# Optimization experiments

Measured on AMD Instinct MI355X. Metric: run time of the kernel, lower is better.

Reference implementation:

```python
import jax, jax.numpy as jnp
import numpy as np


def setup_inputs() -> dict:
    key = jax.random.key(0)
    k1, k2 = jax.random.split(key)
    B, S, D_IN, D_OUT = 4, 2048, 2048, 8192
    x = jax.random.normal(k1, (B, S, D_IN), dtype=jnp.float32)
    # kaiming_normal_ fan_out, linear: std = 1/sqrt(fan_out)
    weight = jax.random.normal(k2, (D_OUT, D_IN), dtype=jnp.float32) * (1.0 / np.sqrt(D_OUT))
    return {"x": x, "weight": weight}


def reference(x, weight):
    # Per-output-row mean-abs scale, clamped
    scale = jnp.clip(jnp.mean(jnp.abs(weight), axis=1, keepdims=True), 1e-5, None)  # [out, 1]
    w_q = jnp.clip(jnp.round(weight / scale), -1.0, 1.0)  # ternary {-1, 0, 1}
    # STE: value = w_q * scale, gradient flows to weight as identity
    w = weight + jax.lax.stop_gradient(w_q * scale - weight)  # [out, in]
    # F.linear: x @ w.T
    return jnp.einsum('bsi,oi->bso', x, w)
```

## Files before the change

### kernel.cpp

```cpp
#include <hip/hip_runtime.h>
#include <hip/hip_bf16.h>
#include <stdint.h>


typedef float floatx4 __attribute__((ext_vector_type(4)));
typedef __bf16 bf16x8 __attribute__((ext_vector_type(8)));

#define BM 128
#define BN 128
#define BK 32

__global__ __launch_bounds__(256) void quant_weight(
    const float* __restrict__ W, uint16_t* __restrict__ Q,
    float* __restrict__ scale, int K )
{
    const int o = blockIdx.x;
    const int t = threadIdx.x;
    const float* row = W + (size_t)o * K;
    const float4* row4 = (const float4*)row;

    float4 v0 = row4[t];
    float4 v1 = row4[t + 256];
    float s = fabsf(v0.x) + fabsf(v0.y) + fabsf(v0.z) + fabsf(v0.w)
            + fabsf(v1.x) + fabsf(v1.y) + fabsf(v1.z) + fabsf(v1.w);
    #pragma unroll
    for (int off = 32; off; off >>= 1) s += __shfl_down(s, off, 64);

    __shared__ float partial[4];
    __shared__ float inv_sh;
    if ((t & 63) == 0) partial[t >> 6] = s;
    __syncthreads();
    if (t == 0) {
        float tot = partial[0] + partial[1] + partial[2] + partial[3];
        float sc = fmaxf(tot / (float)K, 1e-5f);
        scale[o] = sc;
        inv_sh = 1.0f / sc;
    }
    __syncthreads();
    const float inv = inv_sh;

    uint16_t* qrow = Q + (size_t)o * K;
    float q0[4] = {v0.x, v0.y, v0.z, v0.w};
    float q1[4] = {v1.x, v1.y, v1.z, v1.w};
    ushort4 o0, o1;
    unsigned short* p0 = (unsigned short*)&o0;
    unsigned short* p1 = (unsigned short*)&o1;
    #pragma unroll
    for (int i = 0; i < 4; ++i) {
        float a = fminf(fmaxf(rintf(q0[i] * inv), -1.f), 1.f);
        float b = fminf(fmaxf(rintf(q1[i] * inv), -1.f), 1.f);
        p0[i] = (unsigned short)(__float_as_uint(a) >> 16);
        p1[i] = (unsigned short)(__float_as_uint(b) >> 16);
    }
    ((ushort4*)qrow)[t] = o0;
    ((ushort4*)qrow)[t + 256] = o1;
}

__global__ __launch_bounds__(256) void cvt_bf16(
    const float* __restrict__ X, uint16_t* __restrict__ Y)
{
    const size_t i = (size_t)blockIdx.x * blockDim.x + threadIdx.x;
    const float4* x4 = (const float4*)X;
    float4 a = x4[2 * i];
    float4 b = x4[2 * i + 1];
    float v[8] = {a.x, a.y, a.z, a.w, b.x, b.y, b.z, b.w};
    ushort4 lo, hi;
    unsigned short* pl = (unsigned short*)&lo;
    unsigned short* ph = (unsigned short*)&hi;
    #pragma unroll
    for (int j = 0; j < 4; ++j) {
        unsigned ua = __float_as_uint(v[j]);
        unsigned ub = __float_as_uint(v[j + 4]);
        pl[j] = (unsigned short)((ua + 0x7fffu + ((ua >> 16) & 1u)) >> 16);
        ph[j] = (unsigned short)((ub + 0x7fffu + ((ub >> 16) & 1u)) >> 16);
    }
    ((ushort4*)Y)[2 * i] = lo;
    ((ushort4*)Y)[2 * i + 1] = hi;
}

__device__ inline void gload_lds16(const void* g, void* l) {
    __builtin_amdgcn_global_load_lds(
        (const __attribute__((address_space(1))) void*)g,
        (__attribute__((address_space(3))) void*)l, 16, 0, 0);
}

__global__ __launch_bounds__(256) void gemm_bt_scaled(
    const uint16_t* __restrict__ A,
    const uint16_t* __restrict__ B,
    const float* __restrict__ scale,
    float* __restrict__ C,
    int M, int N, int K)
{
    __shared__ __align__(16) uint16_t sA[BM * BK];
    __shared__ __align__(16) uint16_t sB[BN * BK];

    const int tid  = threadIdx.x;
    const int lane = tid & 63;
    const int wv   = tid >> 6;
    const int wm   = wv & 1;
    const int wn   = wv >> 1;
    const int bm   = blockIdx.y;
    const int bn   = blockIdx.x;
    const int rowA0 = bm * BM;
    const int rowB0 = bn * BN;

    const int lrow  = lane & 15;
    const int kquad = lane >> 4;
    const int aoff0 = (wm * 64 + lrow) * BK + kquad * 8;
    const int boff0 = (wn * 64 + lrow) * BK + kquad * 8;

    floatx4 acc[4][4] = {};

    for (int kk = 0; kk < K; kk += BK) {
        #pragma unroll
        for (int j = 0; j < 2; ++j) {
            int c = tid + 256 * j;
            const uint16_t* ga = A + (size_t)(rowA0 + (c >> 2)) * K + kk + (c & 3) * 8;
            gload_lds16(ga, &sA[c * 8]);
        }
        #pragma unroll
        for (int j = 0; j < 2; ++j) {
            int c = tid + 256 * j;
            const uint16_t* gb = B + (size_t)(rowB0 + (c >> 2)) * K + kk + (c & 3) * 8;
            gload_lds16(gb, &sB[c * 8]);
        }
        __syncthreads();

        bf16x8 af[4], bfr[4];
        #pragma unroll
        for (int mt = 0; mt < 4; ++mt)
            af[mt] = *(const bf16x8*)&sA[aoff0 + mt * 16 * BK];
        #pragma unroll
        for (int nt = 0; nt < 4; ++nt)
            bfr[nt] = *(const bf16x8*)&sB[boff0 + nt * 16 * BK];

        #pragma unroll
        for (int mt = 0; mt < 4; ++mt)
            #pragma unroll
            for (int nt = 0; nt < 4; ++nt)
                acc[mt][nt] = __builtin_amdgcn_mfma_f32_16x16x32_bf16(
                    af[mt], bfr[nt], acc[mt][nt], 0, 0, 0);
        __syncthreads();
    }

    const int colb = rowB0 + wn * 64 + lrow;
    const int rowb = rowA0 + wm * 64 + kquad * 4;
    #pragma unroll
    for (int nt = 0; nt < 4; ++nt) {
        const float sc = scale[colb + nt * 16];
        #pragma unroll
        for (int mt = 0; mt < 4; ++mt) {
            #pragma unroll
            for (int r = 0; r < 4; ++r) {
                C[(size_t)(rowb + mt * 16 + r) * N + colb + nt * 16] =
                    acc[mt][nt][r] * sc;
            }
        }
    }
}

extern "C" void kernel_launch(void* const* d_in, const int* in_sizes, int n_in,
                              void* d_out, int out_size, void* d_ws, size_t ws_size,
                              hipStream_t stream) {
    const float* x = (const float*)d_in[0];
    const float* w = (const float*)d_in[1];
    float* out = (float*)d_out;

    const int M = 8192, K = 2048, N = 8192;

    char* ws = (char*)d_ws;
    float*    scale = (float*)ws;
    uint16_t* Xb    = (uint16_t*)(ws + 32768);
    uint16_t* Qb    = (uint16_t*)(ws + 32768 + (size_t)M * K * 2);

    quant_weight<<<N, 256, 0, stream>>>(w, Qb, scale, K);
    cvt_bf16<<<(M * K / 8) / 256, 256, 0, stream>>>(x, Xb);
    gemm_bt_scaled<<<dim3(N / BN, M / BM), 256, 0, stream>>>(Xb, Qb, scale, out, M, N, K);
}
```

Measured before the change: 662.2 us.

## Swizzle LDS tiles, switch GEMM operands to fp16, restructure quant kernel per wave

Adds an XOR swizzle on the k-chunk index, applied both when filling LDS and when reading it, so that fragment reads from shared memory avoid bank conflicts. Operands switch from bf16 to fp16 and use the fp16 MFMA instruction, which gives x more mantissa bits but a narrower exponent range. The weight quantizer now handles one row per wave and reduces with xor shuffles, which removes the shared-memory reduction and block barriers. The input cast kernel is simplified to a plain per-element fp16 conversion.

```diff
diff --git a/kernel.cpp b/kernel.cpp
--- a/kernel.cpp
+++ b/kernel.cpp
@@ -3,79 +3,58 @@
 #include <stdint.h>
 
 
-typedef float floatx4 __attribute__((ext_vector_type(4)));
-typedef __bf16 bf16x8 __attribute__((ext_vector_type(8)));
+typedef float  floatx4 __attribute__((ext_vector_type(4)));
+typedef _Float16 f16x8 __attribute__((ext_vector_type(8)));
+typedef _Float16 f16x4 __attribute__((ext_vector_type(4)));
 
 #define BM 128
 #define BN 128
 #define BK 32
 
 __global__ __launch_bounds__(256) void quant_weight(
-    const float* __restrict__ W, uint16_t* __restrict__ Q,
+    const float* __restrict__ W, f16x4* __restrict__ Q,
     float* __restrict__ scale, int K )
 {
-    const int o = blockIdx.x;
-    const int t = threadIdx.x;
-    const float* row = W + (size_t)o * K;
-    const float4* row4 = (const float4*)row;
+    const int wave = threadIdx.x >> 6;
+    const int lane = threadIdx.x & 63;
+    const int row  = blockIdx.x * 4 + wave;
 
-    float4 v0 = row4[t];
-    float4 v1 = row4[t + 256];
-    float s = fabsf(v0.x) + fabsf(v0.y) + fabsf(v0.z) + fabsf(v0.w)
-            + fabsf(v1.x) + fabsf(v1.y) + fabsf(v1.z) + fabsf(v1.w);
+    const float4* row4 = (const float4*)(W + (size_t)row * K);
+    float4 v[8];
+    float s = 0.f;
     #pragma unroll
-    for (int off = 32; off; off >>= 1) s += __shfl_down(s, off, 64);
+    for (int i = 0; i < 8; ++i) {
+        v[i] = row4[lane + 64 * i];
+        s += fabsf(v[i].x) + fabsf(v[i].y) + fabsf(v[i].z) + fabsf(v[i].w);
+    }
+    #pragma unroll
+    for (int m = 1; m < 64; m <<= 1) s += __shfl_xor(s, m, 64);
 
-    __shared__ float partial[4];
-    __shared__ float inv_sh;
-    if ((t & 63) == 0) partial[t >> 6] = s;
-    __syncthreads();
-    if (t == 0) {
-        float tot = partial[0] + partial[1] + partial[2] + partial[3];
-        float sc = fmaxf(tot / (float)K, 1e-5f);
-        scale[o] = sc;
-        inv_sh = 1.0f / sc;
+    const float sc  = fmaxf(s / (float)K, 1e-5f);
+    if (lane == 0) scale[row] = sc;
+    const float inv = 1.0f / sc;
+
+    f16x4* qrow = Q + (size_t)row * (K / 4);
+    #pragma unroll
+    for (int i = 0; i < 8; ++i) {
+        float t[4] = {v[i].x, v[i].y, v[i].z, v[i].w};
+        f16x4 o;
+        #pragma unroll
+        for (int j = 0; j < 4; ++j)
+            o[j] = (_Float16)fminf(fmaxf(rintf(t[j] * inv), -1.f), 1.f);
+        qrow[lane + 64 * i] = o;
     }
-    __syncthreads();
-    const float inv = inv_sh;
-
-    uint16_t* qrow = Q + (size_t)o * K;
-    float q0[4] = {v0.x, v0.y, v0.z, v0.w};
-    float q1[4] = {v1.x, v1.y, v1.z, v1.w};
-    ushort4 o0, o1;
-    unsigned short* p0 = (unsigned short*)&o0;
-    unsigned short* p1 = (unsigned short*)&o1;
-    #pragma unroll
-    for (int i = 0; i < 4; ++i) {
-        float a = fminf(fmaxf(rintf(q0[i] * inv), -1.f), 1.f);
-        float b = fminf(fmaxf(rintf(q1[i] * inv), -1.f), 1.f);
-        p0[i] = (unsigned short)(__float_as_uint(a) >> 16);
-        p1[i] = (unsigned short)(__float_as_uint(b) >> 16);
-    }
-    ((ushort4*)qrow)[t] = o0;
-    ((ushort4*)qrow)[t + 256] = o1;
 }
 
-__global__ __launch_bounds__(256) void cvt_bf16(
-    const float* __restrict__ X, uint16_t* __restrict__ Y)
+__global__ __launch_bounds__(256) void cvt_f16(
+    const float4* __restrict__ X, f16x4* __restrict__ Y)
 {
     const size_t i = (size_t)blockIdx.x * blockDim.x + threadIdx.x;
-    const float4* x4 = (const float4*)X;
-    float4 a = x4[2 * i];
-    float4 b = x4[2 * i + 1];
-    float v[8] = {a.x, a.y, a.z, a.w, b.x, b.y, b.z, b.w};
-    ushort4 lo, hi;
-    unsigned short* pl = (unsigned short*)&lo;
-    unsigned short* ph = (unsigned short*)&hi;
-    #pragma unroll
-    for (int j = 0; j < 4; ++j) {
-        unsigned ua = __float_as_uint(v[j]);
-        unsigned ub = __float_as_uint(v[j + 4]);
-        pl[j] = (unsigned short)((ua + 0x7fffu + ((ua >> 16) & 1u)) >> 16);
-        ph[j] = (unsigned short)((ub + 0x7fffu + ((ub >> 16) & 1u)) >> 16);
-    }
-    ((ushort4*)Y)[2 * i] = lo;
-    ((ushort4*)Y)[2 * i + 1] = hi;
+    float4 a = X[i];
+    f16x4 o;
+    o[0] = (_Float16)a.x; o[1] = (_Float16)a.y;
+    o[2] = (_Float16)a.z; o[3] = (_Float16)a.w;
+    Y[i] = o;
 }
 
 __device__ inline void gload_lds16(const void* g, void* l) {
@@ -85,60 +64,65 @@
 }
 
 __global__ __launch_bounds__(256) void gemm_bt_scaled(
-    const uint16_t* __restrict__ A,
-    const uint16_t* __restrict__ B,
+    const _Float16* __restrict__ A,
+    const _Float16* __restrict__ B,
     const float* __restrict__ scale,
     float* __restrict__ C,
     int M, int N, int K)
 {
-    __shared__ __align__(16) uint16_t sA[BM * BK];
-    __shared__ __align__(16) uint16_t sB[BN * BK];
+    __shared__ __align__(16) _Float16 sA[BM * BK];
+    __shared__ __align__(16) _Float16 sB[BN * BK];
 
     const int tid  = threadIdx.x;
     const int lane = tid & 63;
     const int wv   = tid >> 6;
     const int wm   = wv & 1;
     const int wn   = wv >> 1;
-    const int bm   = blockIdx.y;
-    const int bn   = blockIdx.x;
-    const int rowA0 = bm * BM;
-    const int rowB0 = bn * BN;
+    const int rowA0 = blockIdx.y * BM;
+    const int rowB0 = blockIdx.x * BN;
 
     const int lrow  = lane & 15;
     const int kquad = lane >> 4;
-    const int aoff0 = (wm * 64 + lrow) * BK + kquad * 8;
-    const int boff0 = (wn * 64 + lrow) * BK + kquad * 8;
 
     floatx4 acc[4][4] = {};
+
+    int aoff[4], boff[4];
+    #pragma unroll
+    for (int t = 0; t < 4; ++t) {
+        int ra = wm * 64 + t * 16 + lrow;
+        int rb = wn * 64 + t * 16 + lrow;
+        aoff[t] = (ra * 4 + (kquad ^ ((ra >> 1) & 3))) * 8;
+        boff[t] = (rb * 4 + (kquad ^ ((rb >> 1) & 3))) * 8;
+    }
 
     for (int kk = 0; kk < K; kk += BK) {
         #pragma unroll
         for (int j = 0; j < 2; ++j) {
             int c = tid + 256 * j;
-            const uint16_t* ga = A + (size_t)(rowA0 + (c >> 2)) * K + kk + (c & 3) * 8;
-            gload_lds16(ga, &sA[c * 8]);
+            int row = c >> 2;
+            int kc  = (c & 3) ^ ((row >> 1) & 3);
+            gload_lds16(A + (size_t)(rowA0 + row) * K + kk + kc * 8, &sA[c * 8]);
         }
         #pragma unroll
         for (int j = 0; j < 2; ++j) {
             int c = tid + 256 * j;
-            const uint16_t* gb = B + (size_t)(rowB0 + (c >> 2)) * K + kk + (c & 3) * 8;
-            gload_lds16(gb, &sB[c * 8]);
+            int row = c >> 2;
+            int kc  = (c & 3) ^ ((row >> 1) & 3);
+            gload_lds16(B + (size_t)(rowB0 + row) * K + kk + kc * 8, &sB[c * 8]);
         }
         __syncthreads();
 
-        bf16x8 af[4], bfr[4];
+        f16x8 af[4], bfr[4];
         #pragma unroll
-        for (int mt = 0; mt < 4; ++mt)
-            af[mt] = *(const bf16x8*)&sA[aoff0 + mt * 16 * BK];
+        for (int mt = 0; mt < 4; ++mt) af[mt]  = *(const f16x8*)&sA[aoff[mt]];
         #pragma unroll
-        for (int nt = 0; nt < 4; ++nt)
-            bfr[nt] = *(const bf16x8*)&sB[boff0 + nt * 16 * BK];
+        for (int nt = 0; nt < 4; ++nt) bfr[nt] = *(const f16x8*)&sB[boff[nt]];
 
         #pragma unroll
         for (int mt = 0; mt < 4; ++mt)
             #pragma unroll
             for (int nt = 0; nt < 4; ++nt)
-                acc[mt][nt] = __builtin_amdgcn_mfma_f32_16x16x32_bf16(
+                acc[mt][nt] = __builtin_amdgcn_mfma_f32_16x16x32_f16(
                     af[mt], bfr[nt], acc[mt][nt], 0, 0, 0);
         __syncthreads();
     }
@@ -169,11 +153,11 @@
     const int M = 8192, K = 2048, N = 8192;
 
     char* ws = (char*)d_ws;
-    float*    scale = (float*)ws;
-    uint16_t* Xb    = (uint16_t*)(ws + 32768);
-    uint16_t* Qb    = (uint16_t*)(ws + 32768 + (size_t)M * K * 2);
+    float*     scale = (float*)ws;
+    _Float16*  Xh    = (_Float16*)(ws + 32768);
+    _Float16*  Qh    = (_Float16*)(ws + 32768 + (size_t)M * K * 2);
 
-    quant_weight<<<N, 256, 0, stream>>>(w, Qb, scale, K);
-    cvt_bf16<<<(M * K / 8) / 256, 256, 0, stream>>>(x, Xb);
-    gemm_bt_scaled<<<dim3(N / BN, M / BM), 256, 0, stream>>>(Xb, Qb, scale, out, M, N, K);
+    quant_weight<<<N / 4, 256, 0, stream>>>(w, (f16x4*)Qh, scale, K);
+    cvt_f16<<<(M * K / 4) / 256, 256, 0, stream>>>((const float4*)x, (f16x4*)Xh);
+    gemm_bt_scaled<<<dim3(N / BN, M / BM), 256, 0, stream>>>(Xh, Qh, scale, out, M, N, K);
 }
```

Result: no change. 655.1 us (-1.1%).
